# Optimization experiments

Hardware: AMD Instinct MI355X
Metric: run time of the kernel (lower is better)

Reference implementation:

```python
import jax, jax.numpy as jnp
import numpy as np

BN_EPS = 1e-5


def _binarize_act(x):
    # sign(x) forward, clipped STE backward (grad passes where |x|<1)
    xc = jnp.clip(x, -1.0, 1.0)
    return xc + jax.lax.stop_gradient(jnp.sign(x) - xc)


def _binarize_weight(w):
    # XNOR/ReActNet: per-out-channel scale * sign(w); clipped-STE gradient
    scale = jax.lax.stop_gradient(jnp.mean(jnp.abs(w), axis=(1, 2, 3), keepdims=True))
    wc = jnp.clip(w, -1.0, 1.0)
    return wc + jax.lax.stop_gradient(scale * jnp.sign(w) - wc)


def setup_inputs() -> dict:
    key = jax.random.key(0)
    ks = jax.random.split(key, 8)
    B, C, H, W = 64, 64, 56, 56
    P = 64  # planes == inplanes (stride 1, no downsample)
    x = jax.random.normal(ks[0], (B, C, H, W), dtype=jnp.float32)
    bias0 = jnp.zeros((1, C, 1, 1), dtype=jnp.float32)
    w = jax.random.normal(ks[1], (P, C, 3, 3), dtype=jnp.float32) * 0.1
    gamma = jnp.ones((P,), dtype=jnp.float32)
    beta = jnp.zeros((P,), dtype=jnp.float32)
    run_mean = jax.random.normal(ks[2], (P,), dtype=jnp.float32) * 0.1
    run_var = jax.random.uniform(ks[3], (P,), dtype=jnp.float32, minval=0.5, maxval=1.5)
    bias1 = jnp.zeros((1, P, 1, 1), dtype=jnp.float32)
    alpha = jnp.full((P,), 0.25, dtype=jnp.float32)  # PReLU default init
    bias2 = jnp.zeros((1, P, 1, 1), dtype=jnp.float32)
    return {"x": x, "bias0": bias0, "w": w, "gamma": gamma, "beta": beta,
            "run_mean": run_mean, "run_var": run_var, "bias1": bias1,
            "alpha": alpha, "bias2": bias2}


def reference(x, bias0, w, gamma, beta, run_mean, run_var, bias1, alpha, bias2):
    residual = x
    out = x + bias0                      # move0 (LearnableBias)
    out = _binarize_act(out)             # BinAct: sign, clipped STE
    bw = _binarize_weight(w)             # BinConv weight binarization
    out = jax.lax.conv_general_dilated(
        out, bw, window_strides=(1, 1), padding=((1, 1), (1, 1)),
        dimension_numbers=("NCHW", "OIHW", "NCHW"))
    # BatchNorm2d (inference form with running stats)
    inv = gamma / jnp.sqrt(run_var + BN_EPS)
    out = out * inv[None, :, None, None] + (beta - run_mean * inv)[None, :, None, None]
    out = out + residual                 # residual add (downsample is None)
    out = out + bias1                    # move1
    a = alpha[None, :, None, None]
    out = jnp.where(out >= 0, out, a * out)  # PReLU
    out = out + bias2                    # move2
    return out
```

## Files before the change

kernel.cpp:

```cpp
#include <hip/hip_runtime.h>

typedef unsigned long long u64;

#define BATCH 64
#define CH    64
#define HH    56
#define WW    56
#define HW    3136
#define NROWS (BATCH * HH)
#define PBLK  896

__global__ __launch_bounds__(256)
void pack_kernel(const float* __restrict__ x,
                 const float* __restrict__ bias0,
                 const float* __restrict__ w,
                 const float* __restrict__ gamma,
                 const float* __restrict__ beta,
                 const float* __restrict__ rmean,
                 const float* __restrict__ rvar,
                 const float* __restrict__ bias1,
                 const float* __restrict__ alpha,
                 const float* __restrict__ bias2,
                 u64* __restrict__ Spk,
                 u64* __restrict__ wbits,
                 float* __restrict__ kc,
                 float4* __restrict__ c4) {
    const int tid = threadIdx.x;
    const int lane = tid & 63;
    const int wv = tid >> 6;
    const int blk = blockIdx.x;

    if (blk < PBLK) {
        const int row = blk * 4 + wv;
        const float* xp = x + ((size_t)((row / HH) * CH + lane)) * HW + (row % HH) * WW;
        const float bz = bias0[lane];
        u64 mine = 0;
#pragma unroll
        for (int q = 0; q < 14; ++q) {
            float4 v = *(const float4*)(xp + q * 4);
            u64 m0 = __ballot(v.x + bz > 0.f);
            u64 m1 = __ballot(v.y + bz > 0.f);
            u64 m2 = __ballot(v.z + bz > 0.f);
            u64 m3 = __ballot(v.w + bz > 0.f);
            mine = (lane == q * 4 + 0) ? m0 : mine;
            mine = (lane == q * 4 + 1) ? m1 : mine;
            mine = (lane == q * 4 + 2) ? m2 : mine;
            mine = (lane == q * 4 + 3) ? m3 : mine;
        }
        if (lane < WW) Spk[(size_t)row * WW + lane] = mine;
    } else {
        __shared__ float red[4];
        const int p = blk - PBLK;
        const float* wp = w + p * 576;
        float s = 0.f;
        for (int i = tid; i < 576; i += 256) s += fabsf(wp[i]);
#pragma unroll
        for (int off = 32; off > 0; off >>= 1) s += __shfl_down(s, off);
        if (lane == 0) red[wv] = s;
        __syncthreads();

        u64 m[9];
        if (wv == 0) {
#pragma unroll
            for (int t = 0; t < 9; ++t) {
                m[t] = __ballot(wp[lane * 9 + t] > 0.f);
                if (lane == 0) wbits[t * 64 + p] = m[t];
            }
        }
        if (tid == 0) {
            float scale = (red[0] + red[1] + red[2] + red[3]) * (1.0f / 576.0f);
            float inv = gamma[p] * rsqrtf(rvar[p] + 1e-5f);
            float am = scale * inv;
            float bd = beta[p] - rmean[p] * inv + bias1[p];
            float pt[9];
#pragma unroll
            for (int t = 0; t < 9; ++t) pt[t] = (float)__popcll(m[t]);
            const float cL = pt[0] + pt[3] + pt[6];
            const float cR = pt[2] + pt[5] + pt[8];
            const float rT = pt[0] + pt[1] + pt[2];
            const float rB = pt[6] + pt[7] + pt[8];
            float Ci[3][3] = {
                {0.f,      cL,                      cR},
                {rT,       rT + pt[3] + pt[6],      rT + pt[5] + pt[8]},
                {rB,       rB + pt[0] + pt[3],      rB + pt[2] + pt[5]}};
            float nv[3][3] = {{9, 6, 6}, {6, 4, 4}, {6, 4, 4}};
#pragma unroll
            for (int wc = 0; wc < 3; ++wc)
#pragma unroll
                for (int lc = 0; lc < 3; ++lc)
                    kc[wc * 192 + lc * 64 + p] =
                        fmaf(am, 64.f * nv[wc][lc] + 2.f * Ci[wc][lc], bd);
            c4[p] = make_float4(-2.f * am, alpha[p], bias2[p], 0.f);
        }
    }
}

__global__ __launch_bounds__(256, 6)
void conv_pop_kernel(const u64* __restrict__ Spk,
                     const u64* __restrict__ wbits,
                     const float* __restrict__ kc,
                     const float4* __restrict__ c4,
                     const float* __restrict__ x,
                     float* __restrict__ out) {
    __shared__ __align__(16) u64 wsm2[64 * 10];
    __shared__ float kcsm[576];
    __shared__ float4 c4sm[64];

    const int tid = threadIdx.x;
    for (int i = tid; i < 576; i += 256) {
        int p = i / 9, t = i - p * 9;
        wsm2[p * 10 + t] = wbits[t * 64 + p];
        kcsm[i] = kc[i];
    }
    if (tid < 64) c4sm[tid] = c4[tid];
    __syncthreads();

    const int bid = blockIdx.x;
    const int wg = (bid & 7) * 224 + (bid >> 3);
    const int lane = tid & 63;
    const int wv = tid >> 6;
    const int row = wg * 2 + (wv & 1);
    const int ph = (wv >> 1) * 32;
    const int b = row / HH;
    const int h = row - b * HH;
    const int wcol = min(lane, WW - 1);
    const bool active = lane < WW;

    const u64* Sb = Spk + (size_t)b * HW;
    u64 a[9];
#pragma unroll
    for (int t = 0; t < 9; ++t) {
        int dh = t / 3 - 1, dw = t % 3 - 1;
        int hh = h + dh, ww = wcol + dw;
        bool valid = ((unsigned)hh < (unsigned)HH) & ((unsigned)ww < (unsigned)WW);
        int hc = min(max(hh, 0), HH - 1);
        int wc2 = min(max(ww, 0), WW - 1);
        a[t] = Sb[hc * WW + wc2] & (valid ? ~0ull : 0ull);
    }

    const int wclass = (h == 0) ? 1 : (h == HH - 1) ? 2 : 0;
    const float* kp = kcsm + wclass * 192 +
                      ((lane == 0) ? 64 : (lane == WW - 1) ? 128 : 0);

    const size_t xbase = (size_t)b * CH * HW + (size_t)h * WW + wcol;

#pragma unroll 4
    for (int i = 0; i < 32; ++i) {
        const int p = ph + i;
        const u64* wp = wsm2 + p * 10;
        unsigned int P = 0;
#pragma unroll
        for (int t = 0; t < 9; ++t) {
            u64 v = a[t] ^ wp[t];
            P += __popc((unsigned int)v);
            P += __popc((unsigned int)(v >> 32));
        }
        const float4 cc = c4sm[p];
        const float k = kp[p];
        const size_t off = xbase + (size_t)p * HW;
        const float res = x[off];
        float v = fmaf(cc.x, (float)P, k) + res;
        v = v >= 0.f ? v : cc.y * v;
        v += cc.z;
        if (active) out[off] = v;
    }
}

extern "C" void kernel_launch(void* const* d_in, const int* in_sizes, int n_in,
                              void* d_out, int out_size, void* d_ws, size_t ws_size,
                              hipStream_t stream) {
    const float* x     = (const float*)d_in[0];
    const float* bias0 = (const float*)d_in[1];
    const float* w     = (const float*)d_in[2];
    const float* gamma = (const float*)d_in[3];
    const float* beta  = (const float*)d_in[4];
    const float* rmean = (const float*)d_in[5];
    const float* rvar  = (const float*)d_in[6];
    const float* bias1 = (const float*)d_in[7];
    const float* alpha = (const float*)d_in[8];
    const float* bias2 = (const float*)d_in[9];
    float* out = (float*)d_out;

    char* ws = (char*)d_ws;
    u64* wbits = (u64*)ws;
    float* kc  = (float*)(ws + 4608);
    float4* c4 = (float4*)(ws + 8192);
    u64* Spk   = (u64*)(ws + 16384);

    pack_kernel<<<PBLK + 64, 256, 0, stream>>>(
        x, bias0, w, gamma, beta, rmean, rvar, bias1, alpha, bias2,
        Spk, wbits, kc, c4);

    conv_pop_kernel<<<NROWS / 2, 256, 0, stream>>>(Spk, wbits, kc, c4, x, out);
}
```

Before: 44.03 us.

## Fuse activation sign-packing into conv kernel with per-band shared-memory halo

```diff
diff --git a/kernel.cpp b/kernel.cpp
--- a/kernel.cpp
+++ b/kernel.cpp
@@ -7,13 +7,11 @@
 #define HH    56
 #define WW    56
 #define HW    3136
-#define NROWS (BATCH * HH)
-#define PBLK  896
+#define NBAND 14
+#define NBLK  (BATCH * NBAND)
 
 __global__ __launch_bounds__(256)
-void pack_kernel(const float* __restrict__ x,
-                 const float* __restrict__ bias0,
-                 const float* __restrict__ w,
+void fold_kernel(const float* __restrict__ w,
                  const float* __restrict__ gamma,
                  const float* __restrict__ beta,
                  const float* __restrict__ rmean,
@@ -21,133 +19,132 @@
                  const float* __restrict__ bias1,
                  const float* __restrict__ alpha,
                  const float* __restrict__ bias2,
-                 u64* __restrict__ Spk,
                  u64* __restrict__ wbits,
                  float* __restrict__ kc,
                  float4* __restrict__ c4) {
+    __shared__ float red[4];
     const int tid = threadIdx.x;
     const int lane = tid & 63;
     const int wv = tid >> 6;
-    const int blk = blockIdx.x;
+    const int p = blockIdx.x;
+    const float* wp = w + p * 576;
 
-    if (blk < PBLK) {
-        const int row = blk * 4 + wv;
-        const float* xp = x + ((size_t)((row / HH) * CH + lane)) * HW + (row % HH) * WW;
-        const float bz = bias0[lane];
-        u64 mine = 0;
+    float s = 0.f;
+    for (int i = tid; i < 576; i += 256) s += fabsf(wp[i]);
 #pragma unroll
-        for (int q = 0; q < 14; ++q) {
-            float4 v = *(const float4*)(xp + q * 4);
-            u64 m0 = __ballot(v.x + bz > 0.f);
-            u64 m1 = __ballot(v.y + bz > 0.f);
-            u64 m2 = __ballot(v.z + bz > 0.f);
-            u64 m3 = __ballot(v.w + bz > 0.f);
-            mine = (lane == q * 4 + 0) ? m0 : mine;
-            mine = (lane == q * 4 + 1) ? m1 : mine;
-            mine = (lane == q * 4 + 2) ? m2 : mine;
-            mine = (lane == q * 4 + 3) ? m3 : mine;
+    for (int off = 32; off > 0; off >>= 1) s += __shfl_down(s, off);
+    if (lane == 0) red[wv] = s;
+    __syncthreads();
+
+    u64 m[9];
+    if (wv == 0) {
+#pragma unroll
+        for (int t = 0; t < 9; ++t) {
+            m[t] = __ballot(wp[lane * 9 + t] > 0.f);
+            if (lane == 0) wbits[p * 10 + t] = m[t];
         }
-        if (lane < WW) Spk[(size_t)row * WW + lane] = mine;
-    } else {
-        __shared__ float red[4];
-        const int p = blk - PBLK;
-        const float* wp = w + p * 576;
-        float s = 0.f;
-        for (int i = tid; i < 576; i += 256) s += fabsf(wp[i]);
+        if (lane == 0) wbits[p * 10 + 9] = 0;
+    }
+    if (tid == 0) {
+        float scale = (red[0] + red[1] + red[2] + red[3]) * (1.0f / 576.0f);
+        float inv = gamma[p] * rsqrtf(rvar[p] + 1e-5f);
+        float am = scale * inv;
+        float bd = beta[p] - rmean[p] * inv + bias1[p];
+        float pt[9];
 #pragma unroll
-        for (int off = 32; off > 0; off >>= 1) s += __shfl_down(s, off);
-        if (lane == 0) red[wv] = s;
-        __syncthreads();
-
-        u64 m[9];
-        if (wv == 0) {
+        for (int t = 0; t < 9; ++t) pt[t] = (float)__popcll(m[t]);
+        const float cL = pt[0] + pt[3] + pt[6];
+        const float cR = pt[2] + pt[5] + pt[8];
+        const float rT = pt[0] + pt[1] + pt[2];
+        const float rB = pt[6] + pt[7] + pt[8];
+        float Ci[3][3] = {
+            {0.f, cL,                 cR},
+            {rT,  rT + pt[3] + pt[6], rT + pt[5] + pt[8]},
+            {rB,  rB + pt[0] + pt[3], rB + pt[2] + pt[5]}};
+        float nv[3][3] = {{9, 6, 6}, {6, 4, 4}, {6, 4, 4}};
 #pragma unroll
-            for (int t = 0; t < 9; ++t) {
-                m[t] = __ballot(wp[lane * 9 + t] > 0.f);
-                if (lane == 0) wbits[t * 64 + p] = m[t];
-            }
-        }
-        if (tid == 0) {
-            float scale = (red[0] + red[1] + red[2] + red[3]) * (1.0f / 576.0f);
-            float inv = gamma[p] * rsqrtf(rvar[p] + 1e-5f);
-            float am = scale * inv;
-            float bd = beta[p] - rmean[p] * inv + bias1[p];
-            float pt[9];
+        for (int wc = 0; wc < 3; ++wc)
 #pragma unroll
-            for (int t = 0; t < 9; ++t) pt[t] = (float)__popcll(m[t]);
-            const float cL = pt[0] + pt[3] + pt[6];
-            const float cR = pt[2] + pt[5] + pt[8];
-            const float rT = pt[0] + pt[1] + pt[2];
-            const float rB = pt[6] + pt[7] + pt[8];
-            float Ci[3][3] = {
-                {0.f,      cL,                      cR},
-                {rT,       rT + pt[3] + pt[6],      rT + pt[5] + pt[8]},
-                {rB,       rB + pt[0] + pt[3],      rB + pt[2] + pt[5]}};
-            float nv[3][3] = {{9, 6, 6}, {6, 4, 4}, {6, 4, 4}};
-#pragma unroll
-            for (int wc = 0; wc < 3; ++wc)
-#pragma unroll
-                for (int lc = 0; lc < 3; ++lc)
-                    kc[wc * 192 + lc * 64 + p] =
-                        fmaf(am, 64.f * nv[wc][lc] + 2.f * Ci[wc][lc], bd);
-            c4[p] = make_float4(-2.f * am, alpha[p], bias2[p], 0.f);
-        }
+            for (int lc = 0; lc < 3; ++lc)
+                kc[wc * 192 + lc * 64 + p] =
+                    fmaf(am, 64.f * nv[wc][lc] + 2.f * Ci[wc][lc], bd);
+        c4[p] = make_float4(-2.f * am, alpha[p], bias2[p], 0.f);
     }
 }
 
-__global__ __launch_bounds__(256, 6)
-void conv_pop_kernel(const u64* __restrict__ Spk,
-                     const u64* __restrict__ wbits,
-                     const float* __restrict__ kc,
-                     const float4* __restrict__ c4,
-                     const float* __restrict__ x,
-                     float* __restrict__ out) {
-    __shared__ __align__(16) u64 wsm2[64 * 10];
+__global__ __launch_bounds__(512, 6)
+void fused_kernel(const float* __restrict__ x,
+                  const float* __restrict__ bias0,
+                  const u64* __restrict__ wbits,
+                  const float* __restrict__ kc,
+                  const float4* __restrict__ c4,
+                  float* __restrict__ out) {
+    __shared__ __align__(16) u64 Lsgn[6][58];
+    __shared__ __align__(16) u64 wsm[64 * 10];
     __shared__ float kcsm[576];
     __shared__ float4 c4sm[64];
 
     const int tid = threadIdx.x;
-    for (int i = tid; i < 576; i += 256) {
-        int p = i / 9, t = i - p * 9;
-        wsm2[p * 10 + t] = wbits[t * 64 + p];
-        kcsm[i] = kc[i];
+    const int lane = tid & 63;
+    const int wv = tid >> 6;
+
+    for (int i = tid; i < 640; i += 512) wsm[i] = wbits[i];
+    for (int i = tid; i < 576; i += 512) kcsm[i] = kc[i];
+    if (tid < 64) c4sm[tid] = c4[tid];
+
+    const int bid = blockIdx.x;
+    const int wg = (bid & 7) * 112 + (bid >> 3);
+    const int b = wg / NBAND;
+    const int band = wg - b * NBAND;
+    const int r0 = band * 4;
+
+    if (wv < 6) {
+        const int ir = r0 - 1 + wv;
+        const bool rowok = (unsigned)ir < (unsigned)HH;
+        u64 mine = 0;
+        if (rowok) {
+            const float* xp = x + ((size_t)(b * CH + lane)) * HW + ir * WW;
+            const float bz = bias0[lane];
+#pragma unroll
+            for (int q = 0; q < 14; ++q) {
+                float4 v = *(const float4*)(xp + q * 4);
+                u64 m0 = __ballot(v.x + bz > 0.f);
+                u64 m1 = __ballot(v.y + bz > 0.f);
+                u64 m2 = __ballot(v.z + bz > 0.f);
+                u64 m3 = __ballot(v.w + bz > 0.f);
+                mine = (lane == q * 4 + 0) ? m0 : mine;
+                mine = (lane == q * 4 + 1) ? m1 : mine;
+                mine = (lane == q * 4 + 2) ? m2 : mine;
+                mine = (lane == q * 4 + 3) ? m3 : mine;
+            }
+        }
+        if (lane < WW) Lsgn[wv][1 + lane] = mine;
+        else if (lane == 56) Lsgn[wv][0] = 0;
+        else if (lane == 57) Lsgn[wv][57] = 0;
     }
-    if (tid < 64) c4sm[tid] = c4[tid];
     __syncthreads();
 
-    const int bid = blockIdx.x;
-    const int wg = (bid & 7) * 224 + (bid >> 3);
-    const int lane = tid & 63;
-    const int wv = tid >> 6;
-    const int row = wg * 2 + (wv & 1);
-    const int ph = (wv >> 1) * 32;
-    const int b = row / HH;
-    const int h = row - b * HH;
+    const int rl = wv & 3;
+    const int ph = (wv >> 2) << 5;
+    const int h = r0 + rl;
     const int wcol = min(lane, WW - 1);
     const bool active = lane < WW;
 
-    const u64* Sb = Spk + (size_t)b * HW;
     u64 a[9];
 #pragma unroll
-    for (int t = 0; t < 9; ++t) {
-        int dh = t / 3 - 1, dw = t % 3 - 1;
-        int hh = h + dh, ww = wcol + dw;
-        bool valid = ((unsigned)hh < (unsigned)HH) & ((unsigned)ww < (unsigned)WW);
-        int hc = min(max(hh, 0), HH - 1);
-        int wc2 = min(max(ww, 0), WW - 1);
-        a[t] = Sb[hc * WW + wc2] & (valid ? ~0ull : 0ull);
-    }
+    for (int t = 0; t < 9; ++t)
+        a[t] = Lsgn[rl + t / 3][wcol + t % 3];
 
     const int wclass = (h == 0) ? 1 : (h == HH - 1) ? 2 : 0;
-    const float* kp = kcsm + wclass * 192 +
-                      ((lane == 0) ? 64 : (lane == WW - 1) ? 128 : 0);
+    const int lclass = (wcol == 0) ? 1 : (lane == WW - 1) ? 2 : 0;
+    const float* kp = kcsm + wclass * 192 + lclass * 64;
 
     const size_t xbase = (size_t)b * CH * HW + (size_t)h * WW + wcol;
 
 #pragma unroll 4
     for (int i = 0; i < 32; ++i) {
         const int p = ph + i;
-        const u64* wp = wsm2 + p * 10;
+        const u64* wp = wsm + p * 10;
         unsigned int P = 0;
 #pragma unroll
         for (int t = 0; t < 9; ++t) {
@@ -183,13 +180,11 @@
 
     char* ws = (char*)d_ws;
     u64* wbits = (u64*)ws;
-    float* kc  = (float*)(ws + 4608);
+    float* kc  = (float*)(ws + 5120);
     float4* c4 = (float4*)(ws + 8192);
-    u64* Spk   = (u64*)(ws + 16384);
 
-    pack_kernel<<<PBLK + 64, 256, 0, stream>>>(
-        x, bias0, w, gamma, beta, rmean, rvar, bias1, alpha, bias2,
-        Spk, wbits, kc, c4);
+    fold_kernel<<<64, 256, 0, stream>>>(
+        w, gamma, beta, rmean, rvar, bias1, alpha, bias2, wbits, kc, c4);
 
-    conv_pop_kernel<<<NROWS / 2, 256, 0, stream>>>(Spk, wbits, kc, c4, x, out);
+    fused_kernel<<<NBLK, 512, 0, stream>>>(x, bias0, wbits, kc, c4, out);
 }
```

Result: slower. 48.38 us (+9.9%).

## Pad packed activation rows and read weight table via scalar loads

Applied to the files above, without the earlier changes.

```diff
diff --git a/kernel.cpp b/kernel.cpp
--- a/kernel.cpp
+++ b/kernel.cpp
@@ -1,13 +1,15 @@
 #include <hip/hip_runtime.h>
 
 typedef unsigned long long u64;
+typedef unsigned int u32;
 
 #define BATCH 64
 #define CH    64
 #define HH    56
 #define WW    56
 #define HW    3136
-#define NROWS (BATCH * HH)
+#define SROW  64
+#define SIMG  (58 * SROW)
 #define PBLK  896
 
 __global__ __launch_bounds__(256)
@@ -22,9 +24,8 @@
                  const float* __restrict__ alpha,
                  const float* __restrict__ bias2,
                  u64* __restrict__ Spk,
-                 u64* __restrict__ wbits,
-                 float* __restrict__ kc,
-                 float4* __restrict__ c4) {
+                 u64* __restrict__ wtab,
+                 float* __restrict__ kc) {
     const int tid = threadIdx.x;
     const int lane = tid & 63;
     const int wv = tid >> 6;
@@ -32,7 +33,9 @@
 
     if (blk < PBLK) {
         const int row = blk * 4 + wv;
-        const float* xp = x + ((size_t)((row / HH) * CH + lane)) * HW + (row % HH) * WW;
+        const int b = row / HH;
+        const int h = row - b * HH;
+        const float* xp = x + ((size_t)(b * CH + lane)) * HW + h * WW;
         const float bz = bias0[lane];
         u64 mine = 0;
 #pragma unroll
@@ -47,7 +50,12 @@
             mine = (lane == q * 4 + 2) ? m2 : mine;
             mine = (lane == q * 4 + 3) ? m3 : mine;
         }
-        if (lane < WW) Spk[(size_t)row * WW + lane] = mine;
+        u64* sp = Spk + (size_t)b * SIMG + (h + 1) * SROW;
+        if (lane < WW)           sp[1 + lane] = mine;
+        else if (lane == 56)     sp[0] = 0;
+        else if (lane == 57)     sp[57] = 0;
+        if (h == 0 && lane < 58)      Spk[(size_t)b * SIMG + lane] = 0;
+        if (h == HH - 1 && lane < 58) Spk[(size_t)b * SIMG + 57 * SROW + lane] = 0;
     } else {
         __shared__ float red[4];
         const int p = blk - PBLK;
@@ -59,110 +67,104 @@
         if (lane == 0) red[wv] = s;
         __syncthreads();
 
-        u64 m[9];
         if (wv == 0) {
+            u64 m[9];
 #pragma unroll
             for (int t = 0; t < 9; ++t) {
                 m[t] = __ballot(wp[lane * 9 + t] > 0.f);
-                if (lane == 0) wbits[t * 64 + p] = m[t];
+                if (lane == 0) wtab[p * 12 + t] = m[t];
             }
-        }
-        if (tid == 0) {
-            float scale = (red[0] + red[1] + red[2] + red[3]) * (1.0f / 576.0f);
-            float inv = gamma[p] * rsqrtf(rvar[p] + 1e-5f);
-            float am = scale * inv;
-            float bd = beta[p] - rmean[p] * inv + bias1[p];
-            float pt[9];
+            if (lane == 0) {
+                float scale = (red[0] + red[1] + red[2] + red[3]) * (1.0f / 576.0f);
+                float inv = gamma[p] * rsqrtf(rvar[p] + 1e-5f);
+                float am = scale * inv;
+                float bd = beta[p] - rmean[p] * inv + bias1[p];
+                float pt[9];
 #pragma unroll
-            for (int t = 0; t < 9; ++t) pt[t] = (float)__popcll(m[t]);
-            const float cL = pt[0] + pt[3] + pt[6];
-            const float cR = pt[2] + pt[5] + pt[8];
-            const float rT = pt[0] + pt[1] + pt[2];
-            const float rB = pt[6] + pt[7] + pt[8];
-            float Ci[3][3] = {
-                {0.f,      cL,                      cR},
-                {rT,       rT + pt[3] + pt[6],      rT + pt[5] + pt[8]},
-                {rB,       rB + pt[0] + pt[3],      rB + pt[2] + pt[5]}};
-            float nv[3][3] = {{9, 6, 6}, {6, 4, 4}, {6, 4, 4}};
+                for (int t = 0; t < 9; ++t) pt[t] = (float)__popcll(m[t]);
+                const float cL = pt[0] + pt[3] + pt[6];
+                const float cR = pt[2] + pt[5] + pt[8];
+                const float rT = pt[0] + pt[1] + pt[2];
+                const float rB = pt[6] + pt[7] + pt[8];
+                float Ci[3][3] = {
+                    {0.f, cL,                 cR},
+                    {rT,  rT + pt[3] + pt[6], rT + pt[5] + pt[8]},
+                    {rB,  rB + pt[0] + pt[3], rB + pt[2] + pt[5]}};
+                float nv[3][3] = {{9, 6, 6}, {6, 4, 4}, {6, 4, 4}};
 #pragma unroll
-            for (int wc = 0; wc < 3; ++wc)
+                for (int wc = 0; wc < 3; ++wc)
 #pragma unroll
-                for (int lc = 0; lc < 3; ++lc)
-                    kc[wc * 192 + lc * 64 + p] =
-                        fmaf(am, 64.f * nv[wc][lc] + 2.f * Ci[wc][lc], bd);
-            c4[p] = make_float4(-2.f * am, alpha[p], bias2[p], 0.f);
+                    for (int lc = 0; lc < 3; ++lc)
+                        kc[(wc * 3 + lc) * 64 + p] =
+                            fmaf(am, 64.f * nv[wc][lc] + 2.f * Ci[wc][lc], bd);
+                float* wf = (float*)(wtab + p * 12 + 9);
+                wf[0] = -2.f * am;
+                wf[1] = alpha[p];
+                wf[2] = bias2[p];
+                wf[3] = 0.f;
+            }
         }
     }
 }
 
 __global__ __launch_bounds__(256, 6)
-void conv_pop_kernel(const u64* __restrict__ Spk,
-                     const u64* __restrict__ wbits,
-                     const float* __restrict__ kc,
-                     const float4* __restrict__ c4,
-                     const float* __restrict__ x,
-                     float* __restrict__ out) {
-    __shared__ __align__(16) u64 wsm2[64 * 10];
+void conv_kernel(const u64* __restrict__ Spk,
+                 const u64* __restrict__ wtab,
+                 const float* __restrict__ kc,
+                 const float* __restrict__ x,
+                 float* __restrict__ out) {
     __shared__ float kcsm[576];
-    __shared__ float4 c4sm[64];
-
     const int tid = threadIdx.x;
-    for (int i = tid; i < 576; i += 256) {
-        int p = i / 9, t = i - p * 9;
-        wsm2[p * 10 + t] = wbits[t * 64 + p];
-        kcsm[i] = kc[i];
-    }
-    if (tid < 64) c4sm[tid] = c4[tid];
+    for (int i = tid; i < 576; i += 256) kcsm[i] = kc[i];
     __syncthreads();
 
     const int bid = blockIdx.x;
     const int wg = (bid & 7) * 224 + (bid >> 3);
     const int lane = tid & 63;
-    const int wv = tid >> 6;
-    const int row = wg * 2 + (wv & 1);
-    const int ph = (wv >> 1) * 32;
+    const int wvu = __builtin_amdgcn_readfirstlane(tid >> 6);
+    const int row = wg * 2 + (wvu & 1);
+    const int ph = (wvu >> 1) << 5;
     const int b = row / HH;
     const int h = row - b * HH;
-    const int wcol = min(lane, WW - 1);
+    const int wl = min(lane, WW - 1);
     const bool active = lane < WW;
 
-    const u64* Sb = Spk + (size_t)b * HW;
-    u64 a[9];
-#pragma unroll
-    for (int t = 0; t < 9; ++t) {
-        int dh = t / 3 - 1, dw = t % 3 - 1;
-        int hh = h + dh, ww = wcol + dw;
-        bool valid = ((unsigned)hh < (unsigned)HH) & ((unsigned)ww < (unsigned)WW);
-        int hc = min(max(hh, 0), HH - 1);
-        int wc2 = min(max(ww, 0), WW - 1);
-        a[t] = Sb[hc * WW + wc2] & (valid ? ~0ull : 0ull);
-    }
+    const u64* ap = Spk + (size_t)b * SIMG + (h + 1) * SROW + (wl + 1);
+    u64 a0 = ap[-SROW - 1], a1 = ap[-SROW], a2 = ap[-SROW + 1];
+    u64 a3 = ap[-1],        a4 = ap[0],     a5 = ap[1];
+    u64 a6 = ap[SROW - 1],  a7 = ap[SROW],  a8 = ap[SROW + 1];
 
     const int wclass = (h == 0) ? 1 : (h == HH - 1) ? 2 : 0;
-    const float* kp = kcsm + wclass * 192 +
-                      ((lane == 0) ? 64 : (lane == WW - 1) ? 128 : 0);
+    const int lclass = (lane == 0) ? 1 : (lane == WW - 1) ? 2 : 0;
+    const float* kp = kcsm + (wclass * 3 + lclass) * 64 + ph;
 
-    const size_t xbase = (size_t)b * CH * HW + (size_t)h * WW + wcol;
+    size_t off = (size_t)b * CH * HW + (size_t)h * WW + wl + (size_t)ph * HW;
+    const u64* wp = wtab + (size_t)ph * 12;
 
-#pragma unroll 4
+#pragma unroll 2
     for (int i = 0; i < 32; ++i) {
-        const int p = ph + i;
-        const u64* wp = wsm2 + p * 10;
-        unsigned int P = 0;
-#pragma unroll
-        for (int t = 0; t < 9; ++t) {
-            u64 v = a[t] ^ wp[t];
-            P += __popc((unsigned int)v);
-            P += __popc((unsigned int)(v >> 32));
-        }
-        const float4 cc = c4sm[p];
-        const float k = kp[p];
-        const size_t off = xbase + (size_t)p * HW;
+        u32 P = 0;
+        u64 v;
+        v = a0 ^ wp[0]; P += __popc((u32)v); P += __popc((u32)(v >> 32));
+        v = a1 ^ wp[1]; P += __popc((u32)v); P += __popc((u32)(v >> 32));
+        v = a2 ^ wp[2]; P += __popc((u32)v); P += __popc((u32)(v >> 32));
+        v = a3 ^ wp[3]; P += __popc((u32)v); P += __popc((u32)(v >> 32));
+        v = a4 ^ wp[4]; P += __popc((u32)v); P += __popc((u32)(v >> 32));
+        v = a5 ^ wp[5]; P += __popc((u32)v); P += __popc((u32)(v >> 32));
+        v = a6 ^ wp[6]; P += __popc((u32)v); P += __popc((u32)(v >> 32));
+        v = a7 ^ wp[7]; P += __popc((u32)v); P += __popc((u32)(v >> 32));
+        v = a8 ^ wp[8]; P += __popc((u32)v); P += __popc((u32)(v >> 32));
+
+        const float* cf = (const float*)(wp + 9);
+        const float k = kp[i];
         const float res = x[off];
-        float v = fmaf(cc.x, (float)P, k) + res;
-        v = v >= 0.f ? v : cc.y * v;
-        v += cc.z;
-        if (active) out[off] = v;
+        float o = fmaf(cf[0], (float)P, k) + res;
+        o = o >= 0.f ? o : cf[1] * o;
+        o += cf[2];
+        if (active) out[off] = o;
+
+        off += HW;
+        wp += 12;
     }
 }
 
@@ -182,14 +184,13 @@
     float* out = (float*)d_out;
 
     char* ws = (char*)d_ws;
-    u64* wbits = (u64*)ws;
-    float* kc  = (float*)(ws + 4608);
-    float4* c4 = (float4*)(ws + 8192);
-    u64* Spk   = (u64*)(ws + 16384);
+    u64* wtab = (u64*)ws;
+    float* kc = (float*)(ws + 6144);
+    u64* Spk  = (u64*)(ws + 16384);
 
     pack_kernel<<<PBLK + 64, 256, 0, stream>>>(
         x, bias0, w, gamma, beta, rmean, rvar, bias1, alpha, bias2,
-        Spk, wbits, kc, c4);
+        Spk, wtab, kc);
 
-    conv_pop_kernel<<<NROWS / 2, 256, 0, stream>>>(Spk, wbits, kc, c4, x, out);
+    conv_kernel<<<(BATCH * HH) / 2, 256, 0, stream>>>(Spk, wtab, kc, x, out);
 }
```

New measurement: 44.22 us. No clear change (+0.4%).
